# Kernel tuning notes

Measured on AMD Instinct MI355X. Metric: run time of the kernel, lower is better.

## Reference

```python
import jax, jax.numpy as jnp
import numpy as np

B, L, D, H = 8, 1024, 512, 8  # batch, seq, d_model, n_head (per-head dim == d_model)
EPS = 1e-6


def setup_inputs() -> dict:
    key = jax.random.key(0)
    ks = jax.random.split(key, 7)
    s = 1.0 / np.sqrt(D)
    return {
        "q": jax.random.normal(ks[0], (B, L, D), jnp.float32),
        "k": jax.random.normal(ks[1], (B, L, D), jnp.float32),
        "v": jax.random.normal(ks[2], (B, L, D), jnp.float32),
        "w_q": jax.random.normal(ks[3], (D, H * D), jnp.float32) * s,
        "w_k": jax.random.normal(ks[4], (D, H * D), jnp.float32) * s,
        "w_v": jax.random.normal(ks[5], (D, H * D), jnp.float32) * s,
        "w_fc": jax.random.normal(ks[6], (H * D, D), jnp.float32) * (1.0 / np.sqrt(H * D)),
        "ln_gamma": jnp.ones((D,), jnp.float32),
        "ln_beta": jnp.zeros((D,), jnp.float32),
    }


def reference(q, k, v, w_q, w_k, w_v, w_fc, ln_gamma, ln_beta):
    residual = q
    # projections -> (B, H, L, D); dropout is identity in eval mode
    qh = (q @ w_q).reshape(B, L, H, D).transpose(0, 2, 1, 3)
    kh = (k @ w_k).reshape(B, L, H, D).transpose(0, 2, 1, 3)
    vh = (v @ w_v).reshape(B, L, H, D).transpose(0, 2, 1, 3)
    temp = jnp.asarray(D, qh.dtype) ** 0.5
    scores = jnp.einsum("bhqd,bhkd->bhqk", qh / temp, kh)
    attn = jax.nn.softmax(scores, axis=-1)
    ctx = jnp.einsum("bhqk,bhkd->bhqd", attn, vh)
    ctx = ctx.transpose(0, 2, 1, 3).reshape(B, L, H * D)
    out = ctx @ w_fc + residual
    mu = jnp.mean(out, axis=-1, keepdims=True)
    var = jnp.var(out, axis=-1, keepdims=True)
    out = (out - mu) * jax.lax.rsqrt(var + EPS) * ln_gamma + ln_beta
    return out, attn
```

## Files before the change

### kernel.cpp

```cpp
#include <hip/hip_runtime.h>
#include <hip/hip_bf16.h>
#include <math.h>

typedef __bf16 bf16_t;
typedef __bf16 bf16x8 __attribute__((ext_vector_type(8)));
typedef __bf16 bf16x4 __attribute__((ext_vector_type(4)));
typedef float  f32x4  __attribute__((ext_vector_type(4)));

#define B_   8
#define L_   1024
#define D_   512
#define H_   8
#define HD_  4096
#define BL_  8192
#define KOFF 33554432L

__device__ __forceinline__ void gload_lds16(const bf16_t* g, bf16_t* l) {
  __builtin_amdgcn_global_load_lds(
      (const __attribute__((address_space(1))) unsigned int*)g,
      (__attribute__((address_space(3))) unsigned int*)l,
      16, 0, 0);
}

__device__ __forceinline__ void xcd_remap(int& tx, int& ty, int& tz) {
  const int nwg = gridDim.x * gridDim.y * gridDim.z;
  const int lin = blockIdx.x + gridDim.x * (blockIdx.y + gridDim.y * blockIdx.z);
  const int virt = (lin & 7) * (nwg >> 3) + (lin >> 3);
  tx = virt % gridDim.x;
  const int rem = virt / gridDim.x;
  ty = rem % gridDim.y;
  tz = rem / gridDim.y;
}

__global__ void f2b3(const float4* __restrict__ q, const float4* __restrict__ k,
                     const float4* __restrict__ v, bf16x4* __restrict__ qo,
                     bf16x4* __restrict__ ko, bf16x4* __restrict__ vo, int n4) {
  int i = blockIdx.x * blockDim.x + threadIdx.x;
  if (i >= n4) return;
  const float4* s = (blockIdx.y == 0) ? q : (blockIdx.y == 1) ? k : v;
  bf16x4* d = (blockIdx.y == 0) ? qo : (blockIdx.y == 1) ? ko : vo;
  float4 x = s[i];
  bf16x4 o;
  o[0] = (bf16_t)x.x; o[1] = (bf16_t)x.y; o[2] = (bf16_t)x.z; o[3] = (bf16_t)x.w;
  d[i] = o;
}

__global__ void tconv4(const float* __restrict__ wq, const float* __restrict__ wk,
                       const float* __restrict__ wv, const float* __restrict__ wfc,
                       bf16_t* __restrict__ wqT, bf16_t* __restrict__ wkT,
                       bf16_t* __restrict__ wvT, bf16_t* __restrict__ wfT) {
  __shared__ float t[32][33];
  const int z = blockIdx.z;
  const float* s; bf16_t* d; int R, C, c0, r0;
  if (z < 3) {
    s = (z == 0) ? wq : (z == 1) ? wk : wv;
    d = (z == 0) ? wqT : (z == 1) ? wkT : wvT;
    R = D_; C = HD_; c0 = blockIdx.x * 32; r0 = blockIdx.y * 32;
  } else {
    s = wfc; d = wfT;
    R = HD_; C = D_; c0 = blockIdx.y * 32; r0 = blockIdx.x * 32;
  }
  int tx = threadIdx.x, ty = threadIdx.y;
  #pragma unroll
  for (int i = 0; i < 32; i += 8)
    t[ty + i][tx] = s[(long)(r0 + ty + i) * C + c0 + tx];
  __syncthreads();
  #pragma unroll
  for (int i = 0; i < 32; i += 8)
    d[(long)(c0 + ty + i) * R + r0 + tx] = (bf16_t)t[tx][ty + i];
}

#define VM4 asm volatile("s_waitcnt vmcnt(4)" ::: "memory")
#define VM0 asm volatile("s_waitcnt vmcnt(0)" ::: "memory")

#define STG(OP, BUF, KK, TILE) do { \
  const bf16_t* gsrc_ = (OP) ? Bg : Ag; \
  const long gld_ = (OP) ? ldb : lda; \
  bf16_t* lb_ = lds + (BUF)*32768 + (OP)*16384 + (KK)*8192 + wid*512; \
  gload_lds16(gsrc_ + (long)(TILE)*64 + (KK)*32, lb_); \
  gload_lds16(gsrc_ + (long)128*gld_ + (long)(TILE)*64 + (KK)*32, lb_ + 4096); \
} while (0)

#define LDA(I, BUF, KK) (*(const bf16x8*)(lds + (BUF)*32768 + (KK)*8192 + offA[I]))
#define LDB(J, BUF, KK) (*(const bf16x8*)(lds + (BUF)*32768 + 16384 + (KK)*8192 + offB[J]))

#define MM(q, ii, jj) acc[(q)*4+(ii)][(jj)] = \
  __builtin_amdgcn_mfma_f32_16x16x32_bf16(a##ii, b##jj, acc[(q)*4+(ii)][(jj)], 0, 0, 0)

#define PHASE(Q, KK, BUF, STAGE, VM) do { \
  bf16x8 a0, a1, a2, a3; \
  if ((Q) == 0) { b0 = LDB(0,BUF,KK); b1 = LDB(1,BUF,KK); b2 = LDB(2,BUF,KK); b3 = LDB(3,BUF,KK); } \
  a0 = LDA((Q)*4+0,BUF,KK); a1 = LDA((Q)*4+1,BUF,KK); \
  a2 = LDA((Q)*4+2,BUF,KK); a3 = LDA((Q)*4+3,BUF,KK); \
  STAGE; \
  __builtin_amdgcn_s_barrier(); \
  asm volatile("s_waitcnt lgkmcnt(0)" ::: "memory"); \
  __builtin_amdgcn_sched_barrier(0); \
  __builtin_amdgcn_s_setprio(1); \
  MM(Q,0,0); MM(Q,1,0); MM(Q,2,0); MM(Q,3,0); \
  MM(Q,0,1); MM(Q,1,1); MM(Q,2,1); MM(Q,3,1); \
  MM(Q,0,2); MM(Q,1,2); MM(Q,2,2); MM(Q,3,2); \
  MM(Q,0,3); MM(Q,1,3); MM(Q,2,3); MM(Q,3,3); \
  __builtin_amdgcn_s_setprio(0); \
  VM; \
  __builtin_amdgcn_s_barrier(); \
} while (0)

template<int EPI>
__launch_bounds__(512, 2)
__global__ void gemm256(const bf16_t* __restrict__ A, long sAb, long sAh, int lda,
                        const bf16_t* __restrict__ Bt, long sBb, long sBh, int ldb,
                        void* __restrict__ Cv, long sCb, long sCh, int ldc,
                        int K, float scale, void* __restrict__ Cv2)
{
  __shared__ __align__(16) bf16_t lds[65536];
  int tx, ty, tz;
  xcd_remap(tx, ty, tz);
  const int bz = tz, b = bz >> 3, h = bz & 7;
  if (EPI == 4) {
    A += (long)((tx >= 32) ? 2 : (tx >= 16) ? 1 : 0) * sAb;
  } else {
    A += (long)b * sAb + (long)h * sAh;
  }
  Bt += (long)b * sBb + (long)h * sBh;
  const int m0 = ty * 256, n0 = tx * 256;
  const int tid = threadIdx.x, lane = tid & 63, wid = tid >> 6;
  const int wm = wid >> 2, wn = wid & 3;

  const int srow  = tid >> 2;
  const int sslot = (lane & 3) ^ ((tid >> 3) & 3);
  const bf16_t* Ag = A + (long)(m0 + srow) * lda + sslot * 8;
  const bf16_t* Bg = Bt + (long)(n0 + srow) * ldb + sslot * 8;

  int offA[8], offB[4];
  #pragma unroll
  for (int i = 0; i < 8; ++i) {
    const int r = wm * 128 + i * 16 + (lane & 15);
    offA[i] = r * 32 + (((lane >> 4) ^ ((r >> 1) & 3)) * 8);
  }
  #pragma unroll
  for (int j = 0; j < 4; ++j) {
    const int r = wn * 64 + j * 16 + (lane & 15);
    offB[j] = r * 32 + (((lane >> 4) ^ ((r >> 1) & 3)) * 8);
  }

  f32x4 acc[8][4] = {};
  const int ITER = K >> 7;

  STG(0,0,0,0); STG(0,0,1,0); STG(1,0,0,0); STG(1,0,1,0);
  STG(0,1,0,1); STG(1,1,0,1);
  VM4;
  __builtin_amdgcn_s_barrier();

  for (int i = 0; i < ITER; ++i) {
    const int t = 2 * i;
    const bool stg = (i + 1 < ITER);
    bf16x8 b0, b1, b2, b3;
    PHASE(0,0,0, STG(0,1,1,t+1);                , (void)0);
    PHASE(1,0,0, STG(1,1,1,t+1);                , (void)0);
    PHASE(0,1,0, { if (stg) STG(0,0,0,t+2); }   , (void)0);
    PHASE(1,1,0, { if (stg) STG(1,0,0,t+2); }   , { if (stg) { VM4; } else { VM0; } });
    PHASE(0,0,1, { if (stg) STG(0,0,1,t+2); }   , (void)0);
    PHASE(1,0,1, { if (stg) STG(1,0,1,t+2); }   , (void)0);
    PHASE(0,1,1, { if (stg) STG(0,1,0,t+3); }   , (void)0);
    PHASE(1,1,1, { if (stg) STG(1,1,0,t+3); }   , { if (stg) { VM4; } });
  }

  const float sc = (EPI == 4 && tx >= 16) ? 1.0f : scale;
  const long coff = (long)b * sCb + (long)h * sCh;
  #pragma unroll
  for (int i = 0; i < 8; ++i) {
    const int rbase = m0 + wm * 128 + i * 16 + ((lane >> 4) << 2);
    #pragma unroll
    for (int j = 0; j < 4; ++j) {
      const int c = n0 + wn * 64 + j * 16 + (lane & 15);
      if (EPI == 4) {
        if (tx < 32) {
          bf16_t* dst = (bf16_t*)Cv + (tx >= 16 ? KOFF : 0);
          const int cc = c - (tx >= 16 ? 4096 : 0);
          #pragma unroll
          for (int r = 0; r < 4; ++r)
            dst[(long)(rbase + r) * HD_ + cc] = (bf16_t)(acc[i][j][r] * sc);
        } else {
          const int cc = c - 8192;
          const int b2 = rbase >> 10, l2 = rbase & 1023;
          const int h2 = cc >> 9, d2 = cc & 511;
          bf16x4 o4;
          #pragma unroll
          for (int r = 0; r < 4; ++r) o4[r] = (bf16_t)acc[i][j][r];
          *(bf16x4*)((bf16_t*)Cv2 + (long)(b2 * 8 + h2) * D_ * L_ + (long)d2 * L_ + l2) = o4;
        }
      } else {
        #pragma unroll
        for (int r = 0; r < 4; ++r) {
          float vv = acc[i][j][r] * sc;
          long idx = coff + (long)(rbase + r) * ldc + c;
          if (EPI == 0) ((bf16_t*)Cv)[idx] = (bf16_t)vv;
          else          ((float*)Cv)[idx] = vv;
        }
      }
    }
  }
}

template<int BM, int BN, int EPI>
__launch_bounds__(256, 2)
__global__ void gemm_bt(const bf16_t* __restrict__ A, long sAb, long sAh, int lda,
                        const bf16_t* __restrict__ Bt, long sBb, long sBh, int ldb,
                        void* __restrict__ Cv, long sCb, long sCh, int ldc,
                        int K, float scale, const float* __restrict__ res)
{
  constexpr int WN    = (BN == 128) ? 2 : 1;
  constexpr int SPANM = BM / (4 / WN);
  constexpr int MI    = SPANM / 16;
  constexpr int NJ    = 4;
  __shared__ bf16_t sA[BM * 64];
  __shared__ bf16_t sB[BN * 64];
  int tx, ty, tz;
  xcd_remap(tx, ty, tz);
  const int bz = tz, b = bz >> 3, h = bz & 7;
  A  += (long)b * sAb + (long)h * sAh;
  Bt += (long)b * sBb + (long)h * sBh;
  const int m0 = ty * BM, n0 = tx * BN;
  const int tid = threadIdx.x, lane = tid & 63, wid = tid >> 6;
  const int waveM = (WN == 2) ? (wid >> 1) : wid;
  const int waveN = (WN == 2) ? (wid & 1) : 0;
  f32x4 acc[MI][NJ] = {};
  const int srow = wid * 8 + (lane >> 3);
  const int skin = (lane & 7) * 8;
  const bf16_t* Ag = A + (long)(m0 + srow) * lda + skin;
  const bf16_t* Bg = Bt + (long)(n0 + srow) * ldb + skin;
  for (int k0 = 0; k0 < K; k0 += 64) {
    #pragma unroll
    for (int j = 0; j < BM / 32; ++j)
      gload_lds16(Ag + (long)(j * 32) * lda + k0, sA + (j * 4 + wid) * 512);
    #pragma unroll
    for (int j = 0; j < BN / 32; ++j)
      gload_lds16(Bg + (long)(j * 32) * ldb + k0, sB + (j * 4 + wid) * 512);
    __syncthreads();
    #pragma unroll
    for (int kk = 0; kk < 2; ++kk) {
      bf16x8 af[MI], bfr[NJ];
      #pragma unroll
      for (int i = 0; i < MI; ++i)
        af[i]  = *(const bf16x8*)(sA + (waveM * SPANM + i * 16 + (lane & 15)) * 64 + kk * 32 + ((lane >> 4) * 8));
      #pragma unroll
      for (int j = 0; j < NJ; ++j)
        bfr[j] = *(const bf16x8*)(sB + (waveN * 64 + j * 16 + (lane & 15)) * 64 + kk * 32 + ((lane >> 4) * 8));
      #pragma unroll
      for (int i = 0; i < MI; ++i)
        #pragma unroll
        for (int j = 0; j < NJ; ++j)
          acc[i][j] = __builtin_amdgcn_mfma_f32_16x16x32_bf16(af[i], bfr[j], acc[i][j], 0, 0, 0);
    }
    __syncthreads();
  }
  const long coff = (long)b * sCb + (long)h * sCh;
  #pragma unroll
  for (int i = 0; i < MI; ++i) {
    const int rbase = m0 + waveM * SPANM + i * 16 + ((lane >> 4) << 2);
    #pragma unroll
    for (int j = 0; j < NJ; ++j) {
      const int c = n0 + waveN * 64 + j * 16 + (lane & 15);
      #pragma unroll
      for (int r = 0; r < 4; ++r) {
        float v = acc[i][j][r] * scale;
        long idx = coff + (long)(rbase + r) * ldc + c;
        if (EPI == 0)      ((bf16_t*)Cv)[idx] = (bf16_t)v;
        else if (EPI == 1) ((float*)Cv)[idx] = v;
        else               ((float*)Cv)[idx] = v + res[(long)(rbase + r) * ldc + c];
      }
    }
  }
}

__global__ void softmax_bf16(bf16_t* __restrict__ braw, float* __restrict__ attn) {
  const long row = (long)blockIdx.x * 4 + (threadIdx.x >> 6);
  const int lane = threadIdx.x & 63;
  bf16_t* p = braw + row * 1024;
  float* ao = attn + row * 1024;
  float v[16];
  float m = -1e30f;
  #pragma unroll
  for (int j = 0; j < 4; ++j) {
    bf16x4 x = *(const bf16x4*)(p + j * 256 + lane * 4);
    #pragma unroll
    for (int e = 0; e < 4; ++e) {
      v[j * 4 + e] = (float)x[e];
      m = fmaxf(m, v[j * 4 + e]);
    }
  }
  #pragma unroll
  for (int o = 32; o; o >>= 1) m = fmaxf(m, __shfl_xor(m, o));
  float s = 0.f;
  #pragma unroll
  for (int e = 0; e < 16; ++e) { v[e] = __expf(v[e] - m); s += v[e]; }
  #pragma unroll
  for (int o = 32; o; o >>= 1) s += __shfl_xor(s, o);
  const float inv = 1.f / s;
  #pragma unroll
  for (int j = 0; j < 4; ++j) {
    float4 f; bf16x4 o4;
    f.x = v[j*4+0] * inv; f.y = v[j*4+1] * inv;
    f.z = v[j*4+2] * inv; f.w = v[j*4+3] * inv;
    o4[0] = (bf16_t)f.x; o4[1] = (bf16_t)f.y; o4[2] = (bf16_t)f.z; o4[3] = (bf16_t)f.w;
    ((float4*)ao)[j * 64 + lane] = f;
    *(bf16x4*)(p + j * 256 + lane * 4) = o4;
  }
}

__global__ void softmax_rows(float* __restrict__ attn, bf16_t* __restrict__ abf) {
  const long row = (long)blockIdx.x * 4 + (threadIdx.x >> 6);
  const int lane = threadIdx.x & 63;
  float* p = attn + row * 1024;
  float4 v[4];
  float m = -1e30f;
  #pragma unroll
  for (int j = 0; j < 4; ++j) {
    v[j] = ((const float4*)p)[j * 64 + lane];
    m = fmaxf(m, fmaxf(fmaxf(v[j].x, v[j].y), fmaxf(v[j].z, v[j].w)));
  }
  #pragma unroll
  for (int o = 32; o; o >>= 1) m = fmaxf(m, __shfl_xor(m, o));
  float s = 0.f;
  #pragma unroll
  for (int j = 0; j < 4; ++j) {
    v[j].x = expf(v[j].x - m); v[j].y = expf(v[j].y - m);
    v[j].z = expf(v[j].z - m); v[j].w = expf(v[j].w - m);
    s += v[j].x + v[j].y + v[j].z + v[j].w;
  }
  #pragma unroll
  for (int o = 32; o; o >>= 1) s += __shfl_xor(s, o);
  const float inv = 1.f / s;
  bf16x4* ab = (bf16x4*)(abf + row * 1024);
  #pragma unroll
  for (int j = 0; j < 4; ++j) {
    v[j].x *= inv; v[j].y *= inv; v[j].z *= inv; v[j].w *= inv;
    ((float4*)p)[j * 64 + lane] = v[j];
    bf16x4 o4;
    o4[0] = (bf16_t)v[j].x; o4[1] = (bf16_t)v[j].y;
    o4[2] = (bf16_t)v[j].z; o4[3] = (bf16_t)v[j].w;
    ab[j * 64 + lane] = o4;
  }
}

__global__ void ln_rows(float* __restrict__ o, const float* __restrict__ g,
                        const float* __restrict__ be) {
  const long row = (long)blockIdx.x * 4 + (threadIdx.x >> 6);
  const int lane = threadIdx.x & 63;
  float* p = o + row * 512;
  float4 a = ((const float4*)p)[lane];
  float4 b = ((const float4*)p)[lane + 64];
  float s  = a.x + a.y + a.z + a.w + b.x + b.y + b.z + b.w;
  float s2 = a.x*a.x + a.y*a.y + a.z*a.z + a.w*a.w
           + b.x*b.x + b.y*b.y + b.z*b.z + b.w*b.w;
  #pragma unroll
  for (int t = 32; t; t >>= 1) { s += __shfl_xor(s, t); s2 += __shfl_xor(s2, t); }
  const float mu  = s * (1.f / 512.f);
  const float var = s2 * (1.f / 512.f) - mu * mu;
  const float inv = rsqrtf(var + 1e-6f);
  float4 g0 = ((const float4*)g)[lane],  g1 = ((const float4*)g)[lane + 64];
  float4 b0 = ((const float4*)be)[lane], b1 = ((const float4*)be)[lane + 64];
  a.x = (a.x - mu) * inv * g0.x + b0.x;  a.y = (a.y - mu) * inv * g0.y + b0.y;
  a.z = (a.z - mu) * inv * g0.z + b0.z;  a.w = (a.w - mu) * inv * g0.w + b0.w;
  b.x = (b.x - mu) * inv * g1.x + b1.x;  b.y = (b.y - mu) * inv * g1.y + b1.y;
  b.z = (b.z - mu) * inv * g1.z + b1.z;  b.w = (b.w - mu) * inv * g1.w + b1.w;
  ((float4*)p)[lane] = a;
  ((float4*)p)[lane + 64] = b;
}

extern "C" void kernel_launch(void* const* d_in, const int* in_sizes, int n_in,
                              void* d_out, int out_size, void* d_ws, size_t ws_size,
                              hipStream_t stream) {
  const float* q   = (const float*)d_in[0];
  const float* k   = (const float*)d_in[1];
  const float* v   = (const float*)d_in[2];
  const float* wq  = (const float*)d_in[3];
  const float* wk  = (const float*)d_in[4];
  const float* wv  = (const float*)d_in[5];
  const float* wfc = (const float*)d_in[6];
  const float* lng = (const float*)d_in[7];
  const float* lnb = (const float*)d_in[8];

  float* out   = (float*)d_out;
  float* attnf = out + (long)BL_ * D_;

  char* ws = (char*)d_ws;
  const long MB = 1024 * 1024;
  bf16_t* qbf = (bf16_t*)(ws +   0 * MB);
  bf16_t* kbf = (bf16_t*)(ws +   8 * MB);
  bf16_t* vbf = (bf16_t*)(ws +  16 * MB);
  bf16_t* wqT = (bf16_t*)(ws +  24 * MB);
  bf16_t* wkT = (bf16_t*)(ws +  28 * MB);
  bf16_t* wvT = (bf16_t*)(ws +  32 * MB);
  bf16_t* wfT = (bf16_t*)(ws +  36 * MB);
  bf16_t* qh  = (bf16_t*)(ws +  40 * MB);
  bf16_t* kh  = (bf16_t*)(ws + 104 * MB);
  bf16_t* vh  = (bf16_t*)(ws + 168 * MB);
  bf16_t* vhT = (bf16_t*)(ws + 232 * MB);
  bf16_t* ctx = vh;

  const bool fused = (ws_size >= (size_t)(424 * MB));
  bf16_t* braw = (bf16_t*)(ws + 296 * MB);
  bf16_t* abf  = fused ? braw : qh;

  const int n4 = BL_ * D_ / 4;
  f2b3<<<dim3(n4 / 256, 3), 256, 0, stream>>>((const float4*)q, (const float4*)k,
                                              (const float4*)v, (bf16x4*)qbf,
                                              (bf16x4*)kbf, (bf16x4*)vbf, n4);
  tconv4<<<dim3(128, 16, 4), dim3(32, 8), 0, stream>>>(wq, wk, wv, wfc,
                                                       wqT, wkT, wvT, wfT);

  const float qscale = 1.0f / sqrtf((float)D_);
  gemm256<4><<<dim3(48, 32, 1), 512, 0, stream>>>(qbf, 4194304L, 0, D_,
                                                  wqT, 0, 0, D_,
                                                  qh, 0, 0, HD_, D_, qscale, vhT);

  if (fused) {
    gemm256<0><<<dim3(4, 4, B_ * H_), 512, 0, stream>>>(
        qh, (long)L_ * HD_, D_, HD_,
        kh, (long)L_ * HD_, D_, HD_,
        braw, (long)H_ * L_ * L_, (long)L_ * L_, L_, D_, 1.0f, nullptr);
    softmax_bf16<<<dim3(B_ * H_ * L_ / 4), 256, 0, stream>>>(braw, attnf);
  } else {
    gemm256<1><<<dim3(4, 4, B_ * H_), 512, 0, stream>>>(
        qh, (long)L_ * HD_, D_, HD_,
        kh, (long)L_ * HD_, D_, HD_,
        attnf, (long)H_ * L_ * L_, (long)L_ * L_, L_, D_, 1.0f, nullptr);
    softmax_rows<<<dim3(B_ * H_ * L_ / 4), 256, 0, stream>>>(attnf, abf);
  }

  gemm256<0><<<dim3(2, 4, B_ * H_), 512, 0, stream>>>(
      abf, (long)H_ * L_ * L_, (long)L_ * L_, L_,
      vhT, (long)H_ * D_ * L_, (long)D_ * L_, L_,
      ctx, (long)L_ * HD_, D_, HD_, L_, 1.0f, nullptr);

  gemm_bt<128,64,2><<<dim3(8, 64, 1), 256, 0, stream>>>(
      ctx, 0, 0, HD_, wfT, 0, 0, HD_,
      out, 0, 0, D_, HD_, 1.0f, q);

  ln_rows<<<dim3(BL_ / 4), 256, 0, stream>>>(out, lng, lnb);
}
```

Baseline: 558.3 us.

## Merge input conversion and weight transpose kernels; widen softmax and LN stores

Folds the fp32-to-bf16 activation conversion and the weight transpose/convert into a single prep launch with 7 z-slices, which removes one kernel launch and its tail. The softmax switches to 8-wide bf16 loads and stores and writes the fp32 attention output with nontemporal stores. LayerNorm also uses nontemporal stores for its output. Both changes target launch overhead and memory traffic in small bandwidth-bound kernels, but nontemporal stores could hurt if the data is reread soon afterwards.

```diff
diff --git a/kernel.cpp b/kernel.cpp
--- a/kernel.cpp
+++ b/kernel.cpp
@@ -32,35 +32,42 @@
   tz = rem / gridDim.y;
 }
 
-__global__ void f2b3(const float4* __restrict__ q, const float4* __restrict__ k,
+__global__ void prep(const float4* __restrict__ q, const float4* __restrict__ k,
                      const float4* __restrict__ v, bf16x4* __restrict__ qo,
-                     bf16x4* __restrict__ ko, bf16x4* __restrict__ vo, int n4) {
-  int i = blockIdx.x * blockDim.x + threadIdx.x;
-  if (i >= n4) return;
-  const float4* s = (blockIdx.y == 0) ? q : (blockIdx.y == 1) ? k : v;
-  bf16x4* d = (blockIdx.y == 0) ? qo : (blockIdx.y == 1) ? ko : vo;
-  float4 x = s[i];
-  bf16x4 o;
-  o[0] = (bf16_t)x.x; o[1] = (bf16_t)x.y; o[2] = (bf16_t)x.z; o[3] = (bf16_t)x.w;
-  d[i] = o;
-}
-
-__global__ void tconv4(const float* __restrict__ wq, const float* __restrict__ wk,
-                       const float* __restrict__ wv, const float* __restrict__ wfc,
-                       bf16_t* __restrict__ wqT, bf16_t* __restrict__ wkT,
-                       bf16_t* __restrict__ wvT, bf16_t* __restrict__ wfT) {
+                     bf16x4* __restrict__ ko, bf16x4* __restrict__ vo,
+                     const float* __restrict__ wq, const float* __restrict__ wk,
+                     const float* __restrict__ wv, const float* __restrict__ wfc,
+                     bf16_t* __restrict__ wqT, bf16_t* __restrict__ wkT,
+                     bf16_t* __restrict__ wvT, bf16_t* __restrict__ wfT) {
   __shared__ float t[32][33];
   const int z = blockIdx.z;
+  if (z < 3) {
+    const float4* s = (z == 0) ? q : (z == 1) ? k : v;
+    bf16x4* d = (z == 0) ? qo : (z == 1) ? ko : vo;
+    const int tid = threadIdx.y * 32 + threadIdx.x;
+    const int base = (blockIdx.y * 128 + blockIdx.x) * 256 + tid;
+    #pragma unroll
+    for (int o = 0; o < 2; ++o) {
+      const int i = base + o * 524288;
+      float4 x = s[i];
+      bf16x4 oo;
+      oo[0] = (bf16_t)x.x; oo[1] = (bf16_t)x.y;
+      oo[2] = (bf16_t)x.z; oo[3] = (bf16_t)x.w;
+      d[i] = oo;
+    }
+    return;
+  }
+  const int zz = z - 3;
   const float* s; bf16_t* d; int R, C, c0, r0;
-  if (z < 3) {
-    s = (z == 0) ? wq : (z == 1) ? wk : wv;
-    d = (z == 0) ? wqT : (z == 1) ? wkT : wvT;
+  if (zz < 3) {
+    s = (zz == 0) ? wq : (zz == 1) ? wk : wv;
+    d = (zz == 0) ? wqT : (zz == 1) ? wkT : wvT;
     R = D_; C = HD_; c0 = blockIdx.x * 32; r0 = blockIdx.y * 32;
   } else {
     s = wfc; d = wfT;
     R = HD_; C = D_; c0 = blockIdx.y * 32; r0 = blockIdx.x * 32;
   }
-  int tx = threadIdx.x, ty = threadIdx.y;
+  const int tx = threadIdx.x, ty = threadIdx.y;
   #pragma unroll
   for (int i = 0; i < 32; i += 8)
     t[ty + i][tx] = s[(long)(r0 + ty + i) * C + c0 + tx];
@@ -282,12 +289,12 @@
   float v[16];
   float m = -1e30f;
   #pragma unroll
-  for (int j = 0; j < 4; ++j) {
-    bf16x4 x = *(const bf16x4*)(p + j * 256 + lane * 4);
-    #pragma unroll
-    for (int e = 0; e < 4; ++e) {
-      v[j * 4 + e] = (float)x[e];
-      m = fmaxf(m, v[j * 4 + e]);
+  for (int j = 0; j < 2; ++j) {
+    bf16x8 x = *(const bf16x8*)(p + j * 512 + lane * 8);
+    #pragma unroll
+    for (int e = 0; e < 8; ++e) {
+      v[j * 8 + e] = (float)x[e];
+      m = fmaxf(m, v[j * 8 + e]);
     }
   }
   #pragma unroll
@@ -299,13 +306,19 @@
   for (int o = 32; o; o >>= 1) s += __shfl_xor(s, o);
   const float inv = 1.f / s;
   #pragma unroll
-  for (int j = 0; j < 4; ++j) {
-    float4 f; bf16x4 o4;
-    f.x = v[j*4+0] * inv; f.y = v[j*4+1] * inv;
-    f.z = v[j*4+2] * inv; f.w = v[j*4+3] * inv;
-    o4[0] = (bf16_t)f.x; o4[1] = (bf16_t)f.y; o4[2] = (bf16_t)f.z; o4[3] = (bf16_t)f.w;
-    ((float4*)ao)[j * 64 + lane] = f;
-    *(bf16x4*)(p + j * 256 + lane * 4) = o4;
+  for (int j = 0; j < 2; ++j) {
+    bf16x8 o8;
+    f32x4 f0, f1;
+    f0[0] = v[j*8+0] * inv; f0[1] = v[j*8+1] * inv;
+    f0[2] = v[j*8+2] * inv; f0[3] = v[j*8+3] * inv;
+    f1[0] = v[j*8+4] * inv; f1[1] = v[j*8+5] * inv;
+    f1[2] = v[j*8+6] * inv; f1[3] = v[j*8+7] * inv;
+    o8[0] = (bf16_t)f0[0]; o8[1] = (bf16_t)f0[1]; o8[2] = (bf16_t)f0[2]; o8[3] = (bf16_t)f0[3];
+    o8[4] = (bf16_t)f1[0]; o8[5] = (bf16_t)f1[1]; o8[6] = (bf16_t)f1[2]; o8[7] = (bf16_t)f1[3];
+    f32x4* a4 = (f32x4*)(ao + j * 512 + lane * 8);
+    __builtin_nontemporal_store(f0, a4);
+    __builtin_nontemporal_store(f1, a4 + 1);
+    *(bf16x8*)(p + j * 512 + lane * 8) = o8;
   }
 }
 
@@ -349,24 +362,25 @@
   const long row = (long)blockIdx.x * 4 + (threadIdx.x >> 6);
   const int lane = threadIdx.x & 63;
   float* p = o + row * 512;
-  float4 a = ((const float4*)p)[lane];
-  float4 b = ((const float4*)p)[lane + 64];
-  float s  = a.x + a.y + a.z + a.w + b.x + b.y + b.z + b.w;
-  float s2 = a.x*a.x + a.y*a.y + a.z*a.z + a.w*a.w
-           + b.x*b.x + b.y*b.y + b.z*b.z + b.w*b.w;
+  f32x4 a = ((const f32x4*)p)[lane];
+  f32x4 b = ((const f32x4*)p)[lane + 64];
+  float s  = a[0] + a[1] + a[2] + a[3] + b[0] + b[1] + b[2] + b[3];
+  float s2 = a[0]*a[0] + a[1]*a[1] + a[2]*a[2] + a[3]*a[3]
+           + b[0]*b[0] + b[1]*b[1] + b[2]*b[2] + b[3]*b[3];
   #pragma unroll
   for (int t = 32; t; t >>= 1) { s += __shfl_xor(s, t); s2 += __shfl_xor(s2, t); }
   const float mu  = s * (1.f / 512.f);
   const float var = s2 * (1.f / 512.f) - mu * mu;
   const float inv = rsqrtf(var + 1e-6f);
-  float4 g0 = ((const float4*)g)[lane],  g1 = ((const float4*)g)[lane + 64];
-  float4 b0 = ((const float4*)be)[lane], b1 = ((const float4*)be)[lane + 64];
-  a.x = (a.x - mu) * inv * g0.x + b0.x;  a.y = (a.y - mu) * inv * g0.y + b0.y;
-  a.z = (a.z - mu) * inv * g0.z + b0.z;  a.w = (a.w - mu) * inv * g0.w + b0.w;
-  b.x = (b.x - mu) * inv * g1.x + b1.x;  b.y = (b.y - mu) * inv * g1.y + b1.y;
-  b.z = (b.z - mu) * inv * g1.z + b1.z;  b.w = (b.w - mu) * inv * g1.w + b1.w;
-  ((float4*)p)[lane] = a;
-  ((float4*)p)[lane + 64] = b;
+  f32x4 g0 = ((const f32x4*)g)[lane],  g1 = ((const f32x4*)g)[lane + 64];
+  f32x4 b0 = ((const f32x4*)be)[lane], b1 = ((const f32x4*)be)[lane + 64];
+  #pragma unroll
+  for (int e = 0; e < 4; ++e) {
+    a[e] = (a[e] - mu) * inv * g0[e] + b0[e];
+    b[e] = (b[e] - mu) * inv * g1[e] + b1[e];
+  }
+  __builtin_nontemporal_store(a, (f32x4*)p + lane);
+  __builtin_nontemporal_store(b, (f32x4*)p + lane + 64);
 }
 
 extern "C" void kernel_launch(void* const* d_in, const int* in_sizes, int n_in,
@@ -404,12 +418,10 @@
   bf16_t* braw = (bf16_t*)(ws + 296 * MB);
   bf16_t* abf  = fused ? braw : qh;
 
-  const int n4 = BL_ * D_ / 4;
-  f2b3<<<dim3(n4 / 256, 3), 256, 0, stream>>>((const float4*)q, (const float4*)k,
-                                              (const float4*)v, (bf16x4*)qbf,
-                                              (bf16x4*)kbf, (bf16x4*)vbf, n4);
-  tconv4<<<dim3(128, 16, 4), dim3(32, 8), 0, stream>>>(wq, wk, wv, wfc,
-                                                       wqT, wkT, wvT, wfT);
+  prep<<<dim3(128, 16, 7), dim3(32, 8), 0, stream>>>(
+      (const float4*)q, (const float4*)k, (const float4*)v,
+      (bf16x4*)qbf, (bf16x4*)kbf, (bf16x4*)vbf,
+      wq, wk, wv, wfc, wqT, wkT, wvT, wfT);
 
   const float qscale = 1.0f / sqrtf((float)D_);
   gemm256<4><<<dim3(48, 32, 1), 512, 0, stream>>>(qbf, 4194304L, 0, D_,
```

Result: slower. 580.4 us (+4.0%).
